# Performance work log

Measured on AMD Instinct MI355X. Metric: run time of the kernel, lower is better.

The kernel has to match this reference:

```python
import jax, jax.numpy as jnp
import numpy as np

EPS = 1e-5      # BatchNorm eps
SLOPE = 0.2     # LeakyReLU negative slope
K = 20          # hardcoded k in Net
OUT_CH = 64     # AGConv out_channels
IN_CH = 6       # AGConv in_channels (= 2*3)


def _bn(x, gamma, beta, axis):
    # Inference-mode BatchNorm: running_mean=0, running_var=1
    shape = [1] * x.ndim
    shape[axis] = -1
    scale = (gamma / jnp.sqrt(1.0 + EPS)).reshape(shape)
    return x * scale + beta.reshape(shape)


def _lrelu(x):
    return jnp.where(x >= 0, x, SLOPE * x)


def _graph_feature(x, k):
    # x: (B, C, N) -> feature (B, 2C, N, k) as in get_graph_feature
    B, C, N = x.shape
    xt = jnp.swapaxes(x, 1, 2)                        # (B, N, C)
    inner = -2.0 * jnp.einsum('bci,bcj->bij', x, x)   # (B, N, N)
    xx = jnp.sum(x * x, axis=1)                       # (B, N)
    pd = -xx[:, :, None] - inner - xx[:, None, :]     # -||xi-xj||^2
    idx = jax.lax.top_k(pd, k)[1]                     # (B, N, k) nearest neighbors
    b_idx = jnp.arange(B)[:, None, None]
    nbr = xt[b_idx, idx]                              # (B, N, k, C) gather
    center = jnp.broadcast_to(xt[:, :, None, :], nbr.shape)
    feat = jnp.concatenate([nbr - center, center], axis=-1)  # (B, N, k, 2C)
    return jnp.moveaxis(feat, -1, 1)                  # (B, 2C, N, k)


def setup_inputs() -> dict:
    key = jax.random.key(0)
    ks = jax.random.split(key, 5)
    B, N = 4, 4096
    x = jax.random.normal(ks[0], (B, 3, N), dtype=jnp.float32)
    w0 = jax.random.normal(ks[1], (OUT_CH, IN_CH), dtype=jnp.float32) * 0.2
    w1 = jax.random.normal(ks[2], (OUT_CH * IN_CH, OUT_CH), dtype=jnp.float32) * 0.05
    w_out = jax.random.normal(ks[3], (3, OUT_CH), dtype=jnp.float32) * 0.1
    return {
        'x': x,
        'w0': w0, 'g0': jnp.ones(OUT_CH), 'b0': jnp.zeros(OUT_CH),
        'w1': w1, 'g1': jnp.ones(OUT_CH), 'b1': jnp.zeros(OUT_CH),
        'w_out': w_out, 'g_out': jnp.ones(3), 'b_out': jnp.zeros(3),
    }


def reference(x, w0, g0, b0, w1, g1, b1, w_out, g_out, b_out):
    # x: (B, 3, N). feat == both `x` and `p` in the torch code (points is x,
    # same idx), so compute once.
    feat = _graph_feature(x, K)                       # (B, 6, N, k)
    B, _, N, k = feat.shape
    # AGConv: weight-generating branch
    y = jnp.einsum('oc,bcnk->bonk', w0, feat)         # conv0 1x1
    y = _lrelu(_bn(y, g0, b0, 1))
    y = jnp.einsum('oc,bcnk->bonk', w1, y)            # conv1 1x1 -> (B, 384, N, k)
    y = jnp.moveaxis(y, 1, -1).reshape(B, N, k, OUT_CH, IN_CH)
    xg = jnp.moveaxis(feat, 1, -1)                    # (B, N, k, 6)
    z = jnp.einsum('bnkoc,bnkc->bnko', y, xg)         # per-edge dynamic matmul
    z = jnp.moveaxis(z, -1, 1)                        # (B, 64, N, k)
    z = _lrelu(_bn(z, g1, b1, 1))
    x1 = jnp.max(z, axis=-1)                          # max over neighbors -> (B, 64, N)
    out = jnp.einsum('oc,bcn->bon', w_out, x1)        # Net.conv1 1x1
    out = _lrelu(_bn(out, g_out, b_out, 1))
    return out
```

## Files before the change

kernel.cpp:

```cpp
#include <hip/hip_runtime.h>
#include <hip/hip_bf16.h>

#define NPTS 4096
#define BATCH 4
#define KNN 20

typedef __attribute__((ext_vector_type(8))) short bf16x8;
typedef __attribute__((ext_vector_type(4))) float f32x4;
typedef __attribute__((ext_vector_type(4))) int i32x4;
typedef unsigned long long u64;

#define OFF_W0S   0
#define OFF_B0F   384
#define OFF_S1F   448
#define OFF_B1F   512
#define OFF_WOUTS 576
#define OFF_BOUTF 768
#define OFF_WHI_BYTES 4096
#define OFF_WLO_BYTES 53248
#define OFF_IDX_BYTES 102400
#define OFF_XQ_BYTES  757760

__device__ __forceinline__ u64 shflx64(u64 v, int off) {
  int lo = __shfl_xor((int)(v & 0xFFFFFFFFull), off);
  int hi = __shfl_xor((int)(v >> 32), off);
  return ((u64)(unsigned)hi << 32) | (unsigned)lo;
}
__device__ __forceinline__ u64 shflbc64(u64 v, int src) {
  int lo = __shfl((int)(v & 0xFFFFFFFFull), src);
  int hi = __shfl((int)(v >> 32), src);
  return ((u64)(unsigned)hi << 32) | (unsigned)lo;
}

__global__ __launch_bounds__(256) void prep_kernel(
    const float* __restrict__ x,
    const float* __restrict__ w0, const float* __restrict__ g0, const float* __restrict__ b0,
    const float* __restrict__ w1, const float* __restrict__ g1, const float* __restrict__ b1,
    const float* __restrict__ wout, const float* __restrict__ gout, const float* __restrict__ bout,
    float* __restrict__ wsf, unsigned short* __restrict__ whi, unsigned short* __restrict__ wlo,
    float4* __restrict__ xq) {
  const float rs = 1.0f / sqrtf(1.0f + 1e-5f);
  int t = blockIdx.x * 256 + threadIdx.x;
  if (t < 384) wsf[OFF_W0S + t] = w0[t] * (g0[t / 6] * rs);
  if (t < 64) {
    wsf[OFF_B0F + t] = b0[t];
    wsf[OFF_S1F + t] = g1[t] * rs;
    wsf[OFF_B1F + t] = b1[t];
  }
  if (t < 192) wsf[OFF_WOUTS + t] = wout[t] * (gout[t / 64] * rs);
  if (t < 3) wsf[OFF_BOUTF + t] = bout[t];
  if (t < BATCH * NPTS) {
    int bb = t >> 12, j = t & (NPTS - 1);
    const float* xb = x + bb * 3 * NPTS;
    float x0 = xb[j], x1 = xb[NPTS + j], x2 = xb[2 * NPTS + j];
    float xx = x0 * x0 + x1 * x1 + x2 * x2;
    xq[t] = make_float4(x0, x1, x2, xx);
  }
  if (t < 24576) {
    int j = t & 7, L = (t >> 3) & 63, ft = t >> 9;
    int kk = ft >> 2, nt = ft & 3;
    int k = kk * 32 + ((L >> 4) << 3) + j;
    int c = k >> 6, d = k & 63;
    int o = nt * 16 + (L & 15);
    float w = w1[(o * 6 + c) * 64 + d];
    unsigned bw = __float_as_uint(w);
    unsigned hb = bw & 0xFFFF0000u;
    float r = w - __uint_as_float(hb);
    whi[t] = (unsigned short)(bw >> 16);
    wlo[t] = (unsigned short)(__float_as_uint(r) >> 16);
  }
}

__global__ __launch_bounds__(64, 4) void knn_kernel(const float4* __restrict__ xq,
                                                    unsigned short* __restrict__ idxbuf) {
  const int pt = blockIdx.x;
  const int b = pt >> 12, n = pt & (NPTS - 1);
  const int lane = threadIdx.x;
  const float4* xqb = xq + b * NPTS;
  const float4 xin = xqb[n];
  const float xi0 = xin.x, xi1 = xin.y, xi2 = xin.z;
  const float nxxi = -xin.w;

  u64 k1 = 0, k2 = 0;
  unsigned lo = 4095u - (unsigned)lane;
#pragma unroll 4
  for (int s = 0; s < 64; ++s) {
    float4 q = xqb[s * 64 + lane];
    float dot = xi0 * q.x + xi1 * q.y + xi2 * q.z;
    float inner = -2.0f * dot;
    float pd = (nxxi - inner) - q.w;
    u64 k = ((u64)(~__float_as_uint(pd)) << 32) | lo;
    lo -= 64u;
    bool c1 = k > k1;
    bool c2 = k > k2;
    u64 t = c1 ? k1 : k;
    k2 = c2 ? t : k2;
    k1 = c1 ? k : k1;
  }

  u64 tk = 0;
  unsigned myout = 0;
#pragma unroll 1
  for (int r = 0; r < KNN; ++r) {
    u64 bk = k1;
    for (int off = 32; off > 0; off >>= 1) {
      u64 ok = shflx64(bk, off);
      if (ok > bk) bk = ok;
    }
    unsigned bj = 4095u - (unsigned)(bk & 4095u);
    if (lane == r) myout = bj;
    bool owner = (k1 == bk);
    u64 bit = 1ull << (bj >> 6);
    if (owner) {
      tk |= bit;
      k1 = k2;
      k2 = 0;
    }
    bool need = owner && (k1 == 0);
    u64 nm = __ballot(need);
    if (nm) {
      int LN = __ffsll(nm) - 1;
      int j2 = lane * 64 + LN;
      float4 q = xqb[j2];
      float dot = xi0 * q.x + xi1 * q.y + xi2 * q.z;
      float inner = -2.0f * dot;
      float pd = (nxxi - inner) - q.w;
      u64 kk = ((u64)(~__float_as_uint(pd)) << 32) | (4095u - (unsigned)j2);
      u64 tkl = shflbc64(tk, LN);
      if ((tkl >> lane) & 1) kk = 0;
      u64 w1k = kk;
      for (int off = 32; off > 0; off >>= 1) {
        u64 ok = shflx64(w1k, off);
        if (ok > w1k) w1k = ok;
      }
      u64 kk2 = (kk == w1k) ? 0 : kk;
      u64 w2k = kk2;
      for (int off = 32; off > 0; off >>= 1) {
        u64 ok = shflx64(w2k, off);
        if (ok > w2k) w2k = ok;
      }
      if (lane == LN) { k1 = w1k; k2 = w2k; }
    }
  }
  if (lane < KNN) idxbuf[pt * KNN + lane] = (unsigned short)myout;
}

__global__ __launch_bounds__(64, 2) void mlp_kernel(const float4* __restrict__ xq,
                                                    const float* __restrict__ wsf,
                                                    const unsigned short* __restrict__ whi,
                                                    const unsigned short* __restrict__ wlo,
                                                    const unsigned short* __restrict__ idxbuf,
                                                    float* __restrict__ out) {
  __shared__ float w0l[448];
  __shared__ float v6l[80 * 12];
  __shared__ float pmax[20 * 66];

  const int lane = threadIdx.x;
  const int quad = lane >> 4, l15 = lane & 15;
  const int pt_base = blockIdx.x * 4;

  const i32x4* whp = (const i32x4*)whi;
  const i32x4* wlp = (const i32x4*)wlo;

  i32x4 wh[4], wl[4];
#pragma unroll
  for (int nt = 0; nt < 4; ++nt) {
    wh[nt] = whp[nt * 64 + lane];
    wl[nt] = wlp[nt * 64 + lane];
  }

  for (int i = lane; i < 448; i += 64) w0l[i] = wsf[i];

#pragma unroll
  for (int rep = 0; rep < 2; ++rep) {
    int e = rep * 64 + lane;
    if (e < 80) {
      int p = e / 20, el = e - p * 20;
      int pt = pt_base + p;
      int b = pt >> 12, n = pt & (NPTS - 1);
      float4 xi = xq[b * NPTS + n];
      int jn = idxbuf[pt * KNN + el];
      float4 xj = xq[b * NPTS + jn];
      v6l[e * 12 + 0] = xj.x - xi.x;
      v6l[e * 12 + 1] = xj.y - xi.y;
      v6l[e * 12 + 2] = xj.z - xi.z;
      v6l[e * 12 + 3] = xi.x;
      v6l[e * 12 + 4] = xi.y;
      v6l[e * 12 + 5] = xi.z;
    }
  }
  __syncthreads();

  f32x4 acc[5][4];
#pragma unroll
  for (int t = 0; t < 5; ++t)
#pragma unroll
    for (int nt = 0; nt < 4; ++nt) acc[t][nt] = (f32x4){0.f, 0.f, 0.f, 0.f};

#pragma unroll 1
  for (int hh = 0; hh < 2; ++hh) {
    float v6r[5][6];
#pragma unroll
    for (int t = 0; t < 5; ++t) {
      const float* vr = v6l + (t * 16 + l15) * 12;
      f32x4 a4 = *(const f32x4*)vr;
      v6r[t][0] = a4.x; v6r[t][1] = a4.y; v6r[t][2] = a4.z; v6r[t][3] = a4.w;
      v6r[t][4] = vr[4]; v6r[t][5] = vr[5];
    }
    float hf[5][8];
#pragma unroll
    for (int j = 0; j < 8; ++j) {
      const int d = hh * 32 + quad * 8 + j;
      const float* wr = w0l + d * 6;
      float wc0 = wr[0], wc1 = wr[1], wc2 = wr[2];
      float wc3 = wr[3], wc4 = wr[4], wc5 = wr[5];
      float bb = w0l[384 + d];
#pragma unroll
      for (int t = 0; t < 5; ++t) {
        float a = bb + wc0 * v6r[t][0] + wc1 * v6r[t][1] + wc2 * v6r[t][2]
                     + wc3 * v6r[t][3] + wc4 * v6r[t][4] + wc5 * v6r[t][5];
        hf[t][j] = fmaxf(a, 0.2f * a);
      }
    }

#pragma unroll 1
    for (int cc = 0; cc < 6; ++cc) {
      const int kk = cc * 2 + hh;
      const bool hasnext = !(hh == 1 && cc == 5);
      const int kkn = (cc < 5) ? kk + 2 : 1;
      i32x4 whn[4], wln[4];
      if (hasnext) {
#pragma unroll
        for (int nt = 0; nt < 4; ++nt) {
          whn[nt] = whp[(kkn * 4 + nt) * 64 + lane];
          wln[nt] = wlp[(kkn * 4 + nt) * 64 + lane];
        }
      }
#pragma unroll
      for (int t = 0; t < 5; ++t) {
        float vc = v6l[(t * 16 + l15) * 12 + cc];
        float u0 = vc * hf[t][0], u1 = vc * hf[t][1];
        float u2 = vc * hf[t][2], u3 = vc * hf[t][3];
        float u4 = vc * hf[t][4], u5 = vc * hf[t][5];
        float u6 = vc * hf[t][6], u7 = vc * hf[t][7];
        unsigned ub0 = __float_as_uint(u0), ub1 = __float_as_uint(u1);
        unsigned ub2 = __float_as_uint(u2), ub3 = __float_as_uint(u3);
        unsigned ub4 = __float_as_uint(u4), ub5 = __float_as_uint(u5);
        unsigned ub6 = __float_as_uint(u6), ub7 = __float_as_uint(u7);
        float r0 = u0 - __uint_as_float(ub0 & 0xFFFF0000u);
        float r1 = u1 - __uint_as_float(ub1 & 0xFFFF0000u);
        float r2 = u2 - __uint_as_float(ub2 & 0xFFFF0000u);
        float r3 = u3 - __uint_as_float(ub3 & 0xFFFF0000u);
        float r4 = u4 - __uint_as_float(ub4 & 0xFFFF0000u);
        float r5 = u5 - __uint_as_float(ub5 & 0xFFFF0000u);
        float r6 = u6 - __uint_as_float(ub6 & 0xFFFF0000u);
        float r7 = u7 - __uint_as_float(ub7 & 0xFFFF0000u);
        i32x4 ah, al;
        ah.x = __builtin_amdgcn_perm(ub1, ub0, 0x07060302);
        ah.y = __builtin_amdgcn_perm(ub3, ub2, 0x07060302);
        ah.z = __builtin_amdgcn_perm(ub5, ub4, 0x07060302);
        ah.w = __builtin_amdgcn_perm(ub7, ub6, 0x07060302);
        al.x = __builtin_amdgcn_perm(__float_as_uint(r1), __float_as_uint(r0), 0x07060302);
        al.y = __builtin_amdgcn_perm(__float_as_uint(r3), __float_as_uint(r2), 0x07060302);
        al.z = __builtin_amdgcn_perm(__float_as_uint(r5), __float_as_uint(r4), 0x07060302);
        al.w = __builtin_amdgcn_perm(__float_as_uint(r7), __float_as_uint(r6), 0x07060302);
        bf16x8 ahv = __builtin_bit_cast(bf16x8, ah);
        bf16x8 alv = __builtin_bit_cast(bf16x8, al);
#pragma unroll
        for (int nt = 0; nt < 4; ++nt) {
          bf16x8 bh = __builtin_bit_cast(bf16x8, wh[nt]);
          bf16x8 bl = __builtin_bit_cast(bf16x8, wl[nt]);
          acc[t][nt] = __builtin_amdgcn_mfma_f32_16x16x32_bf16(ahv, bh, acc[t][nt], 0, 0, 0);
          acc[t][nt] = __builtin_amdgcn_mfma_f32_16x16x32_bf16(ahv, bl, acc[t][nt], 0, 0, 0);
          acc[t][nt] = __builtin_amdgcn_mfma_f32_16x16x32_bf16(alv, bh, acc[t][nt], 0, 0, 0);
        }
      }
      if (hasnext) {
#pragma unroll
        for (int nt = 0; nt < 4; ++nt) { wh[nt] = whn[nt]; wl[nt] = wln[nt]; }
      }
    }
  }
  __syncthreads();

  float s1v[4], b1v[4];
#pragma unroll
  for (int nt = 0; nt < 4; ++nt) {
    s1v[nt] = wsf[OFF_S1F + nt * 16 + l15];
    b1v[nt] = wsf[OFF_B1F + nt * 16 + l15];
  }
#pragma unroll
  for (int t = 0; t < 5; ++t) {
#pragma unroll
    for (int nt = 0; nt < 4; ++nt) {
      f32x4 a = acc[t][nt];
      float z0 = a.x * s1v[nt] + b1v[nt]; z0 = fmaxf(z0, 0.2f * z0);
      float z1 = a.y * s1v[nt] + b1v[nt]; z1 = fmaxf(z1, 0.2f * z1);
      float z2 = a.z * s1v[nt] + b1v[nt]; z2 = fmaxf(z2, 0.2f * z2);
      float z3 = a.w * s1v[nt] + b1v[nt]; z3 = fmaxf(z3, 0.2f * z3);
      float m4 = fmaxf(fmaxf(z0, z1), fmaxf(z2, z3));
      pmax[(t * 4 + quad) * 66 + nt * 16 + l15] = m4;
    }
  }
  __syncthreads();

  float woutr[3];
#pragma unroll
  for (int m = 0; m < 3; ++m) woutr[m] = wsf[OFF_WOUTS + m * 64 + lane];
#pragma unroll
  for (int p = 0; p < 4; ++p) {
    float x1 = pmax[(p * 5 + 0) * 66 + lane];
    x1 = fmaxf(x1, pmax[(p * 5 + 1) * 66 + lane]);
    x1 = fmaxf(x1, pmax[(p * 5 + 2) * 66 + lane]);
    x1 = fmaxf(x1, pmax[(p * 5 + 3) * 66 + lane]);
    x1 = fmaxf(x1, pmax[(p * 5 + 4) * 66 + lane]);
    int pt = pt_base + p;
    int b = pt >> 12, n = pt & (NPTS - 1);
#pragma unroll
    for (int m = 0; m < 3; ++m) {
      float part = woutr[m] * x1;
      for (int off = 32; off > 0; off >>= 1) part += __shfl_xor(part, off);
      if (lane == 0) {
        float ov = part + wsf[OFF_BOUTF + m];
        out[(b * 3 + m) * NPTS + n] = fmaxf(ov, 0.2f * ov);
      }
    }
  }
}

extern "C" void kernel_launch(void* const* d_in, const int* in_sizes, int n_in,
                              void* d_out, int out_size, void* d_ws, size_t ws_size,
                              hipStream_t stream) {
  const float* x    = (const float*)d_in[0];
  const float* w0   = (const float*)d_in[1];
  const float* g0   = (const float*)d_in[2];
  const float* b0   = (const float*)d_in[3];
  const float* w1   = (const float*)d_in[4];
  const float* g1   = (const float*)d_in[5];
  const float* b1   = (const float*)d_in[6];
  const float* wout = (const float*)d_in[7];
  const float* gout = (const float*)d_in[8];
  const float* bout = (const float*)d_in[9];
  float* wsf = (float*)d_ws;
  unsigned short* whi = (unsigned short*)((char*)d_ws + OFF_WHI_BYTES);
  unsigned short* wlo = (unsigned short*)((char*)d_ws + OFF_WLO_BYTES);
  unsigned short* idxbuf = (unsigned short*)((char*)d_ws + OFF_IDX_BYTES);
  float4* xq = (float4*)((char*)d_ws + OFF_XQ_BYTES);
  float* out = (float*)d_out;

  prep_kernel<<<96, 256, 0, stream>>>(x, w0, g0, b0, w1, g1, b1, wout, gout, bout,
                                      wsf, whi, wlo, xq);
  knn_kernel<<<BATCH * NPTS, 64, 0, stream>>>(xq, idxbuf);
  mlp_kernel<<<BATCH * NPTS / 4, 64, 0, stream>>>(xq, wsf, whi, wlo, idxbuf, out);
}
```

Before: 189.0 us.

## Share candidate point tiles in LDS across four query waves in kNN kernel

The kNN kernel now runs four query points per 256-thread block. Each block cooperatively stages 1024-point chunks of the candidate array into shared memory, so four waves reuse each global load instead of each wave streaming the whole point set on its own. The distance expression is folded into an fmaf. This cuts global/L2 traffic but adds two block-wide barriers per chunk, and the fmaf can change rounding slightly, which might flip neighbor ties.

```diff
diff --git a/kernel.cpp b/kernel.cpp
--- a/kernel.cpp
+++ b/kernel.cpp
@@ -71,11 +71,14 @@
   }
 }
 
-__global__ __launch_bounds__(64, 4) void knn_kernel(const float4* __restrict__ xq,
-                                                    unsigned short* __restrict__ idxbuf) {
-  const int pt = blockIdx.x;
+__global__ __launch_bounds__(256, 8) void knn_kernel(const float4* __restrict__ xq,
+                                                     unsigned short* __restrict__ idxbuf) {
+  __shared__ float4 tile[1024];
+  const int tid = threadIdx.x;
+  const int wv = tid >> 6;
+  const int lane = tid & 63;
+  const int pt = blockIdx.x * 4 + wv;
   const int b = pt >> 12, n = pt & (NPTS - 1);
-  const int lane = threadIdx.x;
   const float4* xqb = xq + b * NPTS;
   const float4 xin = xqb[n];
   const float xi0 = xin.x, xi1 = xin.y, xi2 = xin.z;
@@ -83,19 +86,28 @@
 
   u64 k1 = 0, k2 = 0;
   unsigned lo = 4095u - (unsigned)lane;
+#pragma unroll 1
+  for (int t = 0; t < 4; ++t) {
+    float4 pre[4];
+#pragma unroll
+    for (int u = 0; u < 4; ++u) pre[u] = xqb[t * 1024 + u * 256 + tid];
+    __syncthreads();
+#pragma unroll
+    for (int u = 0; u < 4; ++u) tile[u * 256 + tid] = pre[u];
+    __syncthreads();
 #pragma unroll 4
-  for (int s = 0; s < 64; ++s) {
-    float4 q = xqb[s * 64 + lane];
-    float dot = xi0 * q.x + xi1 * q.y + xi2 * q.z;
-    float inner = -2.0f * dot;
-    float pd = (nxxi - inner) - q.w;
-    u64 k = ((u64)(~__float_as_uint(pd)) << 32) | lo;
-    lo -= 64u;
-    bool c1 = k > k1;
-    bool c2 = k > k2;
-    u64 t = c1 ? k1 : k;
-    k2 = c2 ? t : k2;
-    k1 = c1 ? k : k1;
+    for (int i = 0; i < 16; ++i) {
+      float4 q = tile[i * 64 + lane];
+      float dot = xi0 * q.x + xi1 * q.y + xi2 * q.z;
+      float pd = fmaf(2.0f, dot, nxxi) - q.w;
+      u64 k = ((u64)(~__float_as_uint(pd)) << 32) | lo;
+      lo -= 64u;
+      bool c1 = k > k1;
+      bool c2 = k > k2;
+      u64 tt = c1 ? k1 : k;
+      k2 = c2 ? tt : k2;
+      k1 = c1 ? k : k1;
+    }
   }
 
   u64 tk = 0;
@@ -123,8 +135,7 @@
       int j2 = lane * 64 + LN;
       float4 q = xqb[j2];
       float dot = xi0 * q.x + xi1 * q.y + xi2 * q.z;
-      float inner = -2.0f * dot;
-      float pd = (nxxi - inner) - q.w;
+      float pd = fmaf(2.0f, dot, nxxi) - q.w;
       u64 kk = ((u64)(~__float_as_uint(pd)) << 32) | (4095u - (unsigned)j2);
       u64 tkl = shflbc64(tk, LN);
       if ((tkl >> lane) & 1) kk = 0;
@@ -350,6 +361,6 @@
 
   prep_kernel<<<96, 256, 0, stream>>>(x, w0, g0, b0, w1, g1, b1, wout, gout, bout,
                                       wsf, whi, wlo, xq);
-  knn_kernel<<<BATCH * NPTS, 64, 0, stream>>>(xq, idxbuf);
+  knn_kernel<<<BATCH * NPTS / 4, 256, 0, stream>>>(xq, idxbuf);
   mlp_kernel<<<BATCH * NPTS / 4, 64, 0, stream>>>(xq, wsf, whi, wlo, idxbuf, out);
 }
```

Result: slower. 213.5 us (+13.0%).
